# Kernel optimization log

Hardware: AMD Instinct MI355X
Metric: run time of the kernel (lower is better)

The kernel has to match this reference:

```python
import jax, jax.numpy as jnp
import numpy as np
import math

L, B, T, E, HQ, HKV, V = 6, 4, 1024, 1024, 16, 4, 32000
D = E // HQ          # head dim = 64
G = HQ // HKV        # group size = 4
EKV = E // G         # kv proj dim = 256


def setup_inputs() -> dict:
    key = jax.random.key(0)
    ks = jax.random.split(key, 16)
    def n(k, shape):
        return jax.random.normal(k, shape, jnp.float32) * 0.02
    return dict(
        idx=jax.random.randint(ks[0], (B, T), 0, V),
        wte=n(ks[1], (V, E)),
        Wq=n(ks[2], (L, E, E)), bq=jnp.zeros((L, E), jnp.float32),
        Wk=n(ks[3], (L, EKV, E)), bk=jnp.zeros((L, EKV), jnp.float32),
        Wv=n(ks[4], (L, EKV, E)), bv=jnp.zeros((L, EKV), jnp.float32),
        Wo=n(ks[5], (L, E, E)), bo=jnp.zeros((L, E), jnp.float32),
        ln1_w=jnp.ones((L, E), jnp.float32), ln1_b=jnp.zeros((L, E), jnp.float32),
        ln2_w=jnp.ones((L, E), jnp.float32), ln2_b=jnp.zeros((L, E), jnp.float32),
        Wfc=n(ks[6], (L, 4 * E, E)), bfc=jnp.zeros((L, 4 * E), jnp.float32),
        Wproj=n(ks[7], (L, E, 4 * E)), bproj=jnp.zeros((L, E), jnp.float32),
        lnf_w=jnp.ones((E,), jnp.float32), lnf_b=jnp.zeros((E,), jnp.float32),
        lm_head=n(ks[8], (V, E)),
    )


def _ln(x, w, b):
    m = x.mean(-1, keepdims=True)
    v = ((x - m) ** 2).mean(-1, keepdims=True)
    return (x - m) * jax.lax.rsqrt(v + 1e-5) * w + b


def _gelu_new(x):
    c = math.sqrt(2.0 / math.pi)
    return 0.5 * x * (1.0 + jnp.tanh(c * (x + 0.044715 * x ** 3)))


def _rope_tables(t, d):
    # positions start at 1; thetas = base^(-2*(i-1)/d), i = 1..d/2
    pos = jnp.arange(1, t + 1, dtype=jnp.float32)
    thetas = 10000.0 ** (-2.0 * jnp.arange(d // 2, dtype=jnp.float32) / d)
    ang = pos[:, None] * thetas                      # [t, d/2]
    cos = jnp.concatenate([jnp.cos(ang)] * 2, -1)    # [t, d]
    sin = jnp.concatenate([jnp.sin(ang)] * 2, -1)
    return cos, sin


def _apply_rope(x, cos, sin):
    # x: [b, h, t, d]; x_cos = x; x_sin = concat(-right, left)
    x1, x2 = x[..., : D // 2], x[..., D // 2:]
    return x * cos + jnp.concatenate([-x2, x1], -1) * sin


def _gpt_forward(idx, wte, Wq, bq, Wk, bk, Wv, bv, Wo, bo,
                 ln1_w, ln1_b, ln2_w, ln2_b, Wfc, bfc, Wproj, bproj,
                 lnf_w, lnf_b, lm_head):
    cos, sin = _rope_tables(T, D)
    mask = jnp.tril(jnp.ones((T, T), bool))          # causal
    scale = 1.0 / math.sqrt(D)
    x = wte[idx]                                     # [B, T, E]
    for l in range(L):
        h = _ln(x, ln1_w[l], ln1_b[l])
        q = (h @ Wq[l].T + bq[l]).reshape(B, T, HQ, D).transpose(0, 2, 1, 3)
        k = (h @ Wk[l].T + bk[l]).reshape(B, T, HKV, D).transpose(0, 2, 1, 3)
        v = (h @ Wv[l].T + bv[l]).reshape(B, T, HKV, D).transpose(0, 2, 1, 3)
        q = _apply_rope(q, cos, sin)
        k = _apply_rope(k, cos, sin)
        q = q.reshape(B, HKV, G, T, D)               # kv-major head grouping
        att = jnp.einsum('bhgqd,bhkd->bhgqk', q, k) * scale
        att = jnp.where(mask, att, -jnp.inf)
        att = jax.nn.softmax(att, axis=-1)
        y = jnp.einsum('bhgqk,bhkd->bhgqd', att, v)
        y = y.transpose(0, 3, 1, 2, 4).reshape(B, T, E)   # b q (h g d)
        x = x + (y @ Wo[l].T + bo[l])
        h2 = _ln(x, ln2_w[l], ln2_b[l])
        ff = _gelu_new(h2 @ Wfc[l].T + bfc[l]) @ Wproj[l].T + bproj[l]
        x = x + ff
    x = _ln(x, lnf_w, lnf_b)
    return x @ lm_head.T                             # [B, T, V] logits


def reference(idx, wte, Wq, bq, Wk, bk, Wv, bv, Wo, bo,
              ln1_w, ln1_b, ln2_w, ln2_b, Wfc, bfc, Wproj, bproj,
              lnf_w, lnf_b, lm_head):
    return _gpt_forward(idx, wte, Wq, bq, Wk, bk, Wv, bv, Wo, bo,
                        ln1_w, ln1_b, ln2_w, ln2_b, Wfc, bfc, Wproj, bproj,
                        lnf_w, lnf_b, lm_head)
```

## Files before the change

### kernel.cpp

```cpp
#include <hip/hip_runtime.h>

#define Lz 6
#define Bz 4
#define Tz 1024
#define Ez 1024
#define HQz 16
#define HKVz 4
#define Dz 64
#define EKVz 256
#define Vz 32000
#define FFz 4096
#define QKVz 1536

typedef __attribute__((ext_vector_type(4))) float f32x4;
typedef __attribute__((ext_vector_type(8))) short short8;
typedef unsigned short ushort_t;

__device__ inline ushort_t f2b(float f) {
  union { float f; unsigned u; } x; x.f = f;
  unsigned r = x.u + 0x7fffu + ((x.u >> 16) & 1u);
  return (ushort_t)(r >> 16);
}
__device__ inline float b2f(ushort_t u) {
  union { unsigned u; float f; } x; x.u = ((unsigned)u) << 16;
  return x.f;
}
__device__ inline unsigned packbf(float lo, float hi) {
  return (unsigned)f2b(lo) | ((unsigned)f2b(hi) << 16);
}

__device__ inline void gload16(const void* g, void* l) {
  __builtin_amdgcn_global_load_lds(
      (const __attribute__((address_space(1))) void*)g,
      (__attribute__((address_space(3))) void*)l, 16, 0, 0);
}

template<int BIAS, int GELU, int WF32>
__global__ __launch_bounds__(512, 2) void gemm_bt256(
    const ushort_t* __restrict__ A, const ushort_t* __restrict__ Bw,
    const float* __restrict__ bias,
    float* __restrict__ Cf, ushort_t* __restrict__ Cb,
    int M, int N, int K)
{
  __shared__ ushort_t sA[2][2][128 * 64];
  __shared__ ushort_t sB[2][2][128 * 64];
  const int tid = threadIdx.x;
  const int lane = tid & 63, wid = tid >> 6;
  const int wr = wid >> 2, wc = wid & 3;
  const int l15 = lane & 15, l4 = lane >> 4;

  const int gx = gridDim.x;
  const int nwg = gx * gridDim.y;
  const int orig = blockIdx.y * gx + blockIdx.x;
  const int qq = nwg >> 3, rr = nwg & 7;
  const int xcd = orig & 7, loc = orig >> 3;
  const int swz = (xcd < rr) ? (xcd * (qq + 1) + loc)
                             : (rr * (qq + 1) + (xcd - rr) * qq + loc);
  const int bm = swz % gx, bn = swz / gx;

  const int NT = K >> 6;

  auto stage = [&](const ushort_t* src, int row_base, int k0, ushort_t* dst) {
#pragma unroll
    for (int i = 0; i < 2; ++i) {
      int s = i * 512 + tid;
      int row = s >> 3, jp = s & 7;
      int jlog = jp ^ (row & 7);
      gload16(src + (size_t)(row_base + row) * K + k0 + jlog * 8, (char*)dst + s * 16);
    }
  };

  stage(A,  bm * 256,       0, &sA[0][0][0]);
  stage(A,  bm * 256 + 128, 0, &sA[0][1][0]);
  stage(Bw, bn * 256,       0, &sB[0][0][0]);
  stage(Bw, bn * 256 + 128, 0, &sB[0][1][0]);
  stage(A,  bm * 256,       64, &sA[1][0][0]);
  stage(A,  bm * 256 + 128, 64, &sA[1][1][0]);
  stage(Bw, bn * 256,       64, &sB[1][0][0]);
  stage(Bw, bn * 256 + 128, 64, &sB[1][1][0]);
  asm volatile("s_waitcnt vmcnt(8)" ::: "memory");
  __builtin_amdgcn_sched_barrier(0);
  __builtin_amdgcn_s_barrier();
  __builtin_amdgcn_sched_barrier(0);

  f32x4 acc[8][4] = {};
  const int axc = l15 & 7;

  for (int t = 0; t < NT; ++t) {
    const int b = t & 1;
    const ushort_t* pA = &sA[b][wr][0];
    const ushort_t* pB = &sB[b][wc >> 1][(wc & 1) * 64 * 64];
    short8 aF[8][2], bF[4][2];

#pragma unroll
    for (int mt = 0; mt < 4; ++mt)
#pragma unroll
      for (int ks = 0; ks < 2; ++ks)
        aF[mt][ks] = *(const short8*)&pA[(mt * 16 + l15) * 64 + (((ks << 2) + l4) ^ axc) * 8];
#pragma unroll
    for (int nt = 0; nt < 4; ++nt)
      bF[nt][0] = *(const short8*)&pB[(nt * 16 + l15) * 64 + (l4 ^ axc) * 8];
    __builtin_amdgcn_s_setprio(1);
#pragma unroll
    for (int mt = 0; mt < 4; ++mt)
#pragma unroll
      for (int nt = 0; nt < 4; ++nt)
        acc[mt][nt] = __builtin_amdgcn_mfma_f32_16x16x32_bf16(aF[mt][0], bF[nt][0], acc[mt][nt], 0, 0, 0);
    __builtin_amdgcn_s_setprio(0);

#pragma unroll
    for (int mt = 4; mt < 8; ++mt)
#pragma unroll
      for (int ks = 0; ks < 2; ++ks)
        aF[mt][ks] = *(const short8*)&pA[(mt * 16 + l15) * 64 + (((ks << 2) + l4) ^ axc) * 8];
#pragma unroll
    for (int nt = 0; nt < 4; ++nt)
      bF[nt][1] = *(const short8*)&pB[(nt * 16 + l15) * 64 + ((4 + l4) ^ axc) * 8];
    __builtin_amdgcn_s_setprio(1);
#pragma unroll
    for (int mt = 0; mt < 4; ++mt)
#pragma unroll
      for (int nt = 0; nt < 4; ++nt)
        acc[mt][nt] = __builtin_amdgcn_mfma_f32_16x16x32_bf16(aF[mt][1], bF[nt][1], acc[mt][nt], 0, 0, 0);
    __builtin_amdgcn_s_setprio(0);

    asm volatile("s_waitcnt lgkmcnt(0)" ::: "memory");
    __builtin_amdgcn_sched_barrier(0);
    __builtin_amdgcn_s_barrier();
    __builtin_amdgcn_sched_barrier(0);

    const bool pf = (t + 2 < NT);
    if (pf) {
      const int k2 = (t + 2) << 6;
      stage(Bw, bn * 256,       k2, &sB[b][0][0]);
      stage(Bw, bn * 256 + 128, k2, &sB[b][1][0]);
    }
    __builtin_amdgcn_s_setprio(1);
#pragma unroll
    for (int mt = 4; mt < 8; ++mt)
#pragma unroll
      for (int nt = 0; nt < 4; ++nt)
        acc[mt][nt] = __builtin_amdgcn_mfma_f32_16x16x32_bf16(aF[mt][0], bF[nt][0], acc[mt][nt], 0, 0, 0);
    __builtin_amdgcn_s_setprio(0);

    if (pf) {
      const int k2 = (t + 2) << 6;
      stage(A, bm * 256,       k2, &sA[b][0][0]);
      stage(A, bm * 256 + 128, k2, &sA[b][1][0]);
    }
    __builtin_amdgcn_s_setprio(1);
#pragma unroll
    for (int mt = 4; mt < 8; ++mt)
#pragma unroll
      for (int nt = 0; nt < 4; ++nt)
        acc[mt][nt] = __builtin_amdgcn_mfma_f32_16x16x32_bf16(aF[mt][1], bF[nt][1], acc[mt][nt], 0, 0, 0);
    __builtin_amdgcn_s_setprio(0);

    if (t + 1 < NT) {
      if (pf) { asm volatile("s_waitcnt vmcnt(8)" ::: "memory"); }
      else    { asm volatile("s_waitcnt vmcnt(0)" ::: "memory"); }
      __builtin_amdgcn_sched_barrier(0);
      __builtin_amdgcn_s_barrier();
      __builtin_amdgcn_sched_barrier(0);
    }
  }

#pragma unroll
  for (int mt = 0; mt < 8; ++mt) {
#pragma unroll
    for (int nt = 0; nt < 4; ++nt) {
      const int col = bn * 256 + wc * 64 + nt * 16 + l15;
#pragma unroll
      for (int i = 0; i < 4; ++i) {
        const int row = bm * 256 + wr * 128 + mt * 16 + l4 * 4 + i;
        float v = acc[mt][nt][i];
        if (BIAS) v += bias[col];
        if (GELU) {
          float x = v;
          v = 0.5f * x * (1.f + tanhf(0.7978845608028654f * (x + 0.044715f * x * x * x)));
        }
        const size_t o = (size_t)row * N + col;
        if (WF32) Cf[o] = v; else Cb[o] = f2b(v);
      }
    }
  }
}

template<int BIAS, int RES, int GELU, int WBF16, int ROPE>
__global__ __launch_bounds__(256) void gemm_bt64(
    const ushort_t* __restrict__ A, const ushort_t* __restrict__ Bw,
    const float* __restrict__ bias, const ushort_t* __restrict__ res,
    ushort_t* __restrict__ Cb, ushort_t* __restrict__ vtb,
    const float2* __restrict__ tab,
    int M, int N, int K)
{
  __shared__ ushort_t sA[2][128 * 64];
  __shared__ ushort_t sB[2][64 * 64];
  const int tid = threadIdx.x;
  const int lane = tid & 63, wid = tid >> 6;
  const int l15 = lane & 15, l4 = lane >> 4;
  const int xr = l15 & 7;

  const int gx = gridDim.x;
  const int nwg = gx * gridDim.y;
  const int orig = blockIdx.y * gx + blockIdx.x;
  const int qq = nwg >> 3, rr = nwg & 7;
  const int xcd = orig & 7, loc = orig >> 3;
  const int swz = (xcd < rr) ? (xcd * (qq + 1) + loc)
                             : (rr * (qq + 1) + (xcd - rr) * qq + loc);
  const int bm = swz % gx, bn = swz / gx;

  f32x4 acc[2][4] = {};
  const int nK = K >> 6;

  auto stageA = [&](int k0, ushort_t* dst) {
#pragma unroll
    for (int i = 0; i < 4; ++i) {
      int s = i * 256 + tid;
      int row = s >> 3, jp = s & 7;
      int jlog = jp ^ (row & 7);
      gload16(A + (size_t)(bm * 128 + row) * K + k0 + jlog * 8, (char*)dst + s * 16);
    }
  };
  auto stageB = [&](int k0, ushort_t* dst) {
#pragma unroll
    for (int i = 0; i < 2; ++i) {
      int s = i * 256 + tid;
      int row = s >> 3, jp = s & 7;
      int jlog = jp ^ (row & 7);
      gload16(Bw + (size_t)(bn * 64 + row) * K + k0 + jlog * 8, (char*)dst + s * 16);
    }
  };

  stageA(0, &sA[0][0]);
  stageB(0, &sB[0][0]);
  __syncthreads();

  int cur = 0;
  for (int kt = 0; kt < nK; ++kt) {
    if (kt + 1 < nK) {
      const int k0 = (kt + 1) << 6;
      stageA(k0, &sA[cur ^ 1][0]);
      stageB(k0, &sB[cur ^ 1][0]);
    }
    short8 aF[2][2], bF[4][2];
#pragma unroll
    for (int mt = 0; mt < 2; ++mt)
#pragma unroll
      for (int ks = 0; ks < 2; ++ks)
        aF[mt][ks] = *(const short8*)&sA[cur][(wid * 32 + mt * 16 + l15) * 64 + (((ks << 2) + l4) ^ xr) * 8];
#pragma unroll
    for (int nt = 0; nt < 4; ++nt)
#pragma unroll
      for (int ks = 0; ks < 2; ++ks)
        bF[nt][ks] = *(const short8*)&sB[cur][(nt * 16 + l15) * 64 + (((ks << 2) + l4) ^ xr) * 8];
#pragma unroll
    for (int mt = 0; mt < 2; ++mt)
#pragma unroll
      for (int nt = 0; nt < 4; ++nt)
#pragma unroll
        for (int ks = 0; ks < 2; ++ks)
          acc[mt][nt] = __builtin_amdgcn_mfma_f32_16x16x32_bf16(aF[mt][ks], bF[nt][ks], acc[mt][nt], 0, 0, 0);
    __syncthreads();
    cur ^= 1;
  }

  if (ROPE) {
    const int col0 = bn * 64;
    const bool isv = (col0 >= 1280);
#pragma unroll
    for (int mt = 0; mt < 2; ++mt) {
      const int row_base = bm * 128 + wid * 32 + mt * 16 + l4 * 4;
      const int bb = row_base >> 10, t0 = row_base & (Tz - 1);
      if (isv) {
#pragma unroll
        for (int nt = 0; nt < 4; ++nt) {
          const int col = col0 + nt * 16 + l15;
          const int cm = col - 1280, hk = cm >> 6, d = cm & 63;
          ushort4 w;
          w.x = f2b(acc[mt][nt][0] + bias[col]);
          w.y = f2b(acc[mt][nt][1] + bias[col]);
          w.z = f2b(acc[mt][nt][2] + bias[col]);
          w.w = f2b(acc[mt][nt][3] + bias[col]);
          *(ushort4*)&vtb[((size_t)(bb * HKVz + hk) * 64 + d) * Tz + t0] = w;
        }
      } else {
#pragma unroll
        for (int i = 0; i < 4; ++i) {
          const int row = row_base + i;
          const int t = row & (Tz - 1);
#pragma unroll
          for (int nt = 0; nt < 2; ++nt) {
            const int col = col0 + nt * 16 + l15;
            const int jj = nt * 16 + l15;
            const float2 cs = tab[t * 32 + jj];
            const float x1 = acc[mt][nt][i] + bias[col];
            const float x2 = acc[mt][nt + 2][i] + bias[col + 32];
            Cb[(size_t)row * N + col]      = f2b(x1 * cs.x - x2 * cs.y);
            Cb[(size_t)row * N + col + 32] = f2b(x2 * cs.x + x1 * cs.y);
          }
        }
      }
    }
    return;
  }

#pragma unroll
  for (int mt = 0; mt < 2; ++mt) {
#pragma unroll
    for (int nt = 0; nt < 4; ++nt) {
      const int col = bn * 64 + nt * 16 + l15;
#pragma unroll
      for (int i = 0; i < 4; ++i) {
        const int row = bm * 128 + wid * 32 + mt * 16 + l4 * 4 + i;
        float v = acc[mt][nt][i];
        if (BIAS) v += bias[col];
        if (GELU) {
          float t = v;
          v = 0.5f * t * (1.f + tanhf(0.7978845608028654f * (t + 0.044715f * t * t * t)));
        }
        const size_t o = (size_t)row * N + col;
        if (RES) v += b2f(res[o]);
        if (WBF16) Cb[o] = f2b(v);
      }
    }
  }
}

__global__ __launch_bounds__(256, 4) void attn_k(
    const ushort_t* __restrict__ qkv, const ushort_t* __restrict__ vt,
    ushort_t* __restrict__ y)
{
  __shared__ ushort_t sK[2][64 * 64];
  __shared__ ushort_t sV[2][64 * 64];
  __shared__ unsigned sPu[4][512];
  const int bh = blockIdx.y;
  const int b = bh >> 4, h = bh & 15, hk = h >> 2;
  const int tid = threadIdx.x, lane = tid & 63, wid = tid >> 6;
  const int l15 = lane & 15, l4 = lane >> 4;
  const int xr = l15 & 7;

  for (int pass = 0; pass < 2; ++pass) {
    const int qt = pass ? (int)blockIdx.x : (Tz / 64 - 1 - (int)blockIdx.x);
    const int qrow0 = qt * 64 + wid * 16;
    const int qg = qrow0 + l15;
    const int ntile = qt + 1;

    short8 aQ[2];
#pragma unroll
    for (int ks = 0; ks < 2; ++ks)
      aQ[ks] = *(const short8*)&qkv[(size_t)(b * Tz + qrow0 + l15) * QKVz + h * 64 + ks * 32 + l4 * 8];

    float m = -1e30f, lsum = 0.f;
    f32x4 o[4] = {};

    if (pass) __syncthreads();

#pragma unroll
    for (int j = 0; j < 2; ++j) {
      int s = wid * 128 + j * 64 + lane;
      int row = s >> 3, jp = s & 7, jlog = jp ^ (row & 7);
      gload16(qkv + (size_t)(b * Tz + row) * QKVz + Ez + hk * 64 + jlog * 8, (char*)&sK[0][0] + s * 16);
      gload16(vt + (size_t)((b * HKVz + hk) * 64 + row) * Tz + jlog * 8, (char*)&sV[0][0] + s * 16);
    }

    for (int t = 0; t < ntile; ++t) {
      asm volatile("s_waitcnt vmcnt(0)" ::: "memory");
      __syncthreads();
      if (t + 1 < ntile) {
        const int nb = (t + 1) & 1;
#pragma unroll
        for (int j = 0; j < 2; ++j) {
          int s = wid * 128 + j * 64 + lane;
          int row = s >> 3, jp = s & 7, jlog = jp ^ (row & 7);
          gload16(qkv + (size_t)(b * Tz + (t + 1) * 64 + row) * QKVz + Ez + hk * 64 + jlog * 8,
                  (char*)&sK[nb][0] + s * 16);
          gload16(vt + (size_t)((b * HKVz + hk) * 64 + row) * Tz + (t + 1) * 64 + jlog * 8,
                  (char*)&sV[nb][0] + s * 16);
        }
      }
      const ushort_t* K = &sK[t & 1][0];
      const ushort_t* V = &sV[t & 1][0];

      f32x4 sacc[4] = {};
#pragma unroll
      for (int nt = 0; nt < 4; ++nt) {
#pragma unroll
        for (int ks = 0; ks < 2; ++ks) {
          short8 aK = *(const short8*)&K[(nt * 16 + l15) * 64 + (((ks << 2) + l4) ^ xr) * 8];
          sacc[nt] = __builtin_amdgcn_mfma_f32_16x16x32_bf16(aK, aQ[ks], sacc[nt], 0, 0, 0);
        }
      }

      float sv[4][4];
      float pmax = -1e30f;
#pragma unroll
      for (int nt = 0; nt < 4; ++nt)
#pragma unroll
        for (int i = 0; i < 4; ++i) {
          int key = t * 64 + nt * 16 + l4 * 4 + i;
          float s = sacc[nt][i] * 0.125f;
          if (key > qg) s = -1e30f;
          sv[nt][i] = s;
          pmax = fmaxf(pmax, s);
        }
      pmax = fmaxf(pmax, __shfl_xor(pmax, 16));
      pmax = fmaxf(pmax, __shfl_xor(pmax, 32));
      const float mnew = fmaxf(m, pmax);
      const float corr = __expf(m - mnew);
      float psum = 0.f;
#pragma unroll
      for (int nt = 0; nt < 4; ++nt)
#pragma unroll
        for (int i = 0; i < 4; ++i) {
          float p = __expf(sv[nt][i] - mnew);
          sv[nt][i] = p;
          psum += p;
        }
      psum += __shfl_xor(psum, 16);
      psum += __shfl_xor(psum, 32);
      lsum = lsum * corr + psum;
      m = mnew;
#pragma unroll
      for (int dt = 0; dt < 4; ++dt) o[dt] *= corr;

#pragma unroll
      for (int nt = 0; nt < 4; ++nt) {
        uint2 u;
        u.x = packbf(sv[nt][0], sv[nt][1]);
        u.y = packbf(sv[nt][2], sv[nt][3]);
        *(uint2*)&sPu[wid][l15 * 32 + (((nt * 2 + (l4 >> 1)) ^ xr) << 2) + ((l4 & 1) << 1)] = u;
      }
      short8 aP[2];
#pragma unroll
      for (int ks = 0; ks < 2; ++ks)
        aP[ks] = *(const short8*)&sPu[wid][l15 * 32 + ((((ks << 2) + l4) ^ xr) << 2)];

#pragma unroll
      for (int dt = 0; dt < 4; ++dt) {
#pragma unroll
        for (int ks = 0; ks < 2; ++ks) {
          short8 aV = *(const short8*)&V[(dt * 16 + l15) * 64 + (((ks << 2) + l4) ^ xr) * 8];
          o[dt] = __builtin_amdgcn_mfma_f32_16x16x32_bf16(aV, aP[ks], o[dt], 0, 0, 0);
        }
      }
    }

    const float inv = 1.f / lsum;
    const size_t yrow = (size_t)(b * Tz + qrow0 + l15) * Ez + h * 64;
#pragma unroll
    for (int dt = 0; dt < 4; ++dt) {
      ushort4 w;
      w.x = f2b(o[dt][0] * inv);
      w.y = f2b(o[dt][1] * inv);
      w.z = f2b(o[dt][2] * inv);
      w.w = f2b(o[dt][3] * inv);
      *(ushort4*)&y[yrow + dt * 16 + l4 * 4] = w;
    }
  }
}

__global__ __launch_bounds__(256) void ln_bf16(
    const ushort_t* __restrict__ x, const float* __restrict__ w,
    const float* __restrict__ b, ushort_t* __restrict__ out)
{
  __shared__ float red[8];
  const int row = blockIdx.x, tid = threadIdx.x;
  ushort4 xv = *(const ushort4*)&x[(size_t)row * Ez + tid * 4];
  float v0 = b2f(xv.x), v1 = b2f(xv.y), v2 = b2f(xv.z), v3 = b2f(xv.w);
  float s = v0 + v1 + v2 + v3;
  float sq = v0 * v0 + v1 * v1 + v2 * v2 + v3 * v3;
#pragma unroll
  for (int off = 1; off < 64; off <<= 1) { s += __shfl_xor(s, off); sq += __shfl_xor(sq, off); }
  if ((tid & 63) == 0) { red[(tid >> 6) * 2] = s; red[(tid >> 6) * 2 + 1] = sq; }
  __syncthreads();
  const float ts = red[0] + red[2] + red[4] + red[6];
  const float tq = red[1] + red[3] + red[5] + red[7];
  const float mean = ts * (1.f / Ez);
  const float var = tq * (1.f / Ez) - mean * mean;
  const float rstd = rsqrtf(var + 1e-5f);
  float4 wv = *(const float4*)&w[tid * 4];
  float4 bv = *(const float4*)&b[tid * 4];
  ushort4 ov;
  ov.x = f2b((v0 - mean) * rstd * wv.x + bv.x);
  ov.y = f2b((v1 - mean) * rstd * wv.y + bv.y);
  ov.z = f2b((v2 - mean) * rstd * wv.z + bv.z);
  ov.w = f2b((v3 - mean) * rstd * wv.w + bv.w);
  *(ushort4*)&out[(size_t)row * Ez + tid * 4] = ov;
}

__global__ __launch_bounds__(256) void embed_k(
    const int* __restrict__ idx, const float* __restrict__ wte, ushort_t* __restrict__ x)
{
  int i = blockIdx.x * 256 + threadIdx.x;
  int row = i >> 8, c = (i & 255) << 2;
  float4 v = *(const float4*)&wte[(size_t)idx[row] * Ez + c];
  ushort4 o;
  o.x = f2b(v.x); o.y = f2b(v.y); o.z = f2b(v.z); o.w = f2b(v.w);
  *(ushort4*)&x[(size_t)row * Ez + c] = o;
}

__global__ __launch_bounds__(256) void cvt_bf16(
    const float* __restrict__ in, ushort_t* __restrict__ out, int n)
{
  int i = (blockIdx.x * 256 + threadIdx.x) * 4;
  if (i >= n) return;
  float4 v = *(const float4*)&in[i];
  ushort4 o;
  o.x = f2b(v.x); o.y = f2b(v.y); o.z = f2b(v.z); o.w = f2b(v.w);
  *(ushort4*)&out[i] = o;
}

__global__ __launch_bounds__(256) void cvt_layer(
    const float* __restrict__ Wq, const float* __restrict__ Wk,
    const float* __restrict__ Wv, const float* __restrict__ Wo_,
    const float* __restrict__ Wfc_, const float* __restrict__ Wpj_,
    ushort_t* __restrict__ wqkv, ushort_t* __restrict__ wo,
    ushort_t* __restrict__ wfc, ushort_t* __restrict__ wpj)
{
  int i = (blockIdx.x * 256 + threadIdx.x) * 4;
  const float* src; ushort_t* dst; int off;
  if (i < 1048576)       { src = Wq;   dst = wqkv;           off = i; }
  else if (i < 1310720)  { src = Wk;   dst = wqkv + 1048576; off = i - 1048576; }
  else if (i < 1572864)  { src = Wv;   dst = wqkv + 1310720; off = i - 1310720; }
  else if (i < 2621440)  { src = Wo_;  dst = wo;             off = i - 1572864; }
  else if (i < 6815744)  { src = Wfc_; dst = wfc;            off = i - 2621440; }
  else                   { src = Wpj_; dst = wpj;            off = i - 6815744; }
  float4 v = *(const float4*)&src[off];
  ushort4 o;
  o.x = f2b(v.x); o.y = f2b(v.y); o.z = f2b(v.z); o.w = f2b(v.w);
  *(ushort4*)&dst[off] = o;
}

__global__ __launch_bounds__(256) void setup_k(
    const float* __restrict__ bq, const float* __restrict__ bk,
    const float* __restrict__ bv, float2* __restrict__ tab, float* __restrict__ qbia)
{
  int i = blockIdx.x * 256 + threadIdx.x;
  int t = i >> 5, j = i & 31;
  float theta = powf(10000.0f, -(float)j / 32.0f);
  float ang = (float)(t + 1) * theta;
  tab[i] = make_float2(cosf(ang), sinf(ang));
  if (i < Lz * QKVz) {
    int l = i / QKVz, jj = i - l * QKVz;
    float v = (jj < Ez) ? bq[l * Ez + jj]
            : ((jj < Ez + EKVz) ? bk[l * EKVz + jj - Ez] : bv[l * EKVz + jj - Ez - EKVz]);
    qbia[i] = v;
  }
}

template<int BIAS, int RES, int GELU, int WBF16, int ROPE = 0>
static void launch_gemm64(const ushort_t* A, const ushort_t* Bw, const float* bias,
                          const ushort_t* res, ushort_t* Cb,
                          ushort_t* vtb, const float* tab,
                          int M, int N, int K, hipStream_t s)
{
  dim3 g(M / 128, N / 64);
  gemm_bt64<BIAS, RES, GELU, WBF16, ROPE><<<g, 256, 0, s>>>(
      A, Bw, bias, res, Cb, vtb, (const float2*)tab, M, N, K);
}

extern "C" void kernel_launch(void* const* d_in, const int* in_sizes, int n_in,
                              void* d_out, int out_size, void* d_ws, size_t ws_size,
                              hipStream_t stream)
{
  (void)in_sizes; (void)n_in; (void)out_size; (void)ws_size;
  const int*   idx   = (const int*)d_in[0];
  const float* wte   = (const float*)d_in[1];
  const float* Wq    = (const float*)d_in[2];
  const float* bq    = (const float*)d_in[3];
  const float* Wk    = (const float*)d_in[4];
  const float* bk    = (const float*)d_in[5];
  const float* Wv    = (const float*)d_in[6];
  const float* bv    = (const float*)d_in[7];
  const float* Wo    = (const float*)d_in[8];
  const float* bo    = (const float*)d_in[9];
  const float* ln1w  = (const float*)d_in[10];
  const float* ln1b  = (const float*)d_in[11];
  const float* ln2w  = (const float*)d_in[12];
  const float* ln2b  = (const float*)d_in[13];
  const float* Wfc   = (const float*)d_in[14];
  const float* bfc   = (const float*)d_in[15];
  const float* Wproj = (const float*)d_in[16];
  const float* bproj = (const float*)d_in[17];
  const float* lnfw  = (const float*)d_in[18];
  const float* lnfb  = (const float*)d_in[19];
  const float* lmh   = (const float*)d_in[20];
  float* out = (float*)d_out;

  char* ws = (char*)d_ws;
  size_t off = 0;
  auto alloc = [&](size_t bytes) -> void* {
    void* p = ws + off;
    off += (bytes + 255) & ~(size_t)255;
    return p;
  };
  ushort_t* wbuf  = (ushort_t*)alloc((size_t)Vz * Ez * 2);
  ushort_t* x     = (ushort_t*)alloc((size_t)Bz * Tz * Ez * 2);
  ushort_t* hb    = (ushort_t*)alloc((size_t)Bz * Tz * Ez * 2);
  ushort_t* qkvb  = (ushort_t*)alloc((size_t)Bz * Tz * QKVz * 2);
  ushort_t* vtb   = (ushort_t*)alloc((size_t)Bz * HKVz * 64 * Tz * 2);
  ushort_t* yb    = (ushort_t*)alloc((size_t)Bz * Tz * Ez * 2);
  ushort_t* ffb   = (ushort_t*)alloc((size_t)Bz * Tz * FFz * 2);
  float*    tab   = (float*)alloc((size_t)Tz * 32 * 2 * 4);
  float*    qbia  = (float*)alloc((size_t)Lz * QKVz * 4);

  ushort_t* wqkv = wbuf;
  ushort_t* wo   = wqkv + (size_t)QKVz * Ez;
  ushort_t* wfc  = wo + (size_t)Ez * Ez;
  ushort_t* wpj  = wfc + (size_t)FFz * Ez;

  const int M = Bz * Tz;

  setup_k<<<Tz * 32 / 256, 256, 0, stream>>>(bq, bk, bv, (float2*)tab, qbia);
  embed_k<<<Bz * Tz, 256, 0, stream>>>(idx, wte, x);

  for (int l = 0; l < Lz; ++l) {
    ln_bf16<<<M, 256, 0, stream>>>(x, ln1w + l * Ez, ln1b + l * Ez, hb);
    cvt_layer<<<10752, 256, 0, stream>>>(
        Wq + (size_t)l * Ez * Ez, Wk + (size_t)l * EKVz * Ez, Wv + (size_t)l * EKVz * Ez,
        Wo + (size_t)l * Ez * Ez, Wfc + (size_t)l * FFz * Ez, Wproj + (size_t)l * Ez * FFz,
        wqkv, wo, wfc, wpj);
    launch_gemm64<1, 0, 0, 1, 1>(hb, wqkv, qbia + l * QKVz, nullptr, qkvb, vtb, tab,
                                 M, QKVz, Ez, stream);
    attn_k<<<dim3(Tz / 128, Bz * HQz), 256, 0, stream>>>(qkvb, vtb, yb);
    launch_gemm64<1, 1, 0, 1>(yb, wo, bo + l * Ez, x, x, nullptr, nullptr,
                              M, Ez, Ez, stream);
    ln_bf16<<<M, 256, 0, stream>>>(x, ln2w + l * Ez, ln2b + l * Ez, hb);
    {
      dim3 g(M / 256, FFz / 256);
      gemm_bt256<1, 1, 0><<<g, 512, 0, stream>>>(hb, wfc, bfc + l * FFz, nullptr, ffb, M, FFz, Ez);
    }
    launch_gemm64<1, 1, 0, 1>(ffb, wpj, bproj + l * Ez, x, x, nullptr, nullptr,
                              M, Ez, FFz, stream);
  }
  ln_bf16<<<M, 256, 0, stream>>>(x, lnfw, lnfb, hb);
  cvt_bf16<<<(Vz * Ez / 4 + 255) / 256, 256, 0, stream>>>(lmh, wbuf, Vz * Ez);
  {
    dim3 g(M / 256, Vz / 256);
    gemm_bt256<0, 0, 1><<<g, 512, 0, stream>>>(hb, wbuf, nullptr, out, nullptr, M, Vz, Ez);
  }
}
```

Baseline: 1.592 ms.

## Load GEMM A fragments directly from global memory, staging only B in LDS

```diff
diff --git a/kernel.cpp b/kernel.cpp
--- a/kernel.cpp
+++ b/kernel.cpp
@@ -36,18 +36,18 @@
 }
 
 template<int BIAS, int GELU, int WF32>
-__global__ __launch_bounds__(512, 2) void gemm_bt256(
+__global__ __launch_bounds__(512, 1) void gemm_bt256(
     const ushort_t* __restrict__ A, const ushort_t* __restrict__ Bw,
     const float* __restrict__ bias,
     float* __restrict__ Cf, ushort_t* __restrict__ Cb,
     int M, int N, int K)
 {
-  __shared__ ushort_t sA[2][2][128 * 64];
   __shared__ ushort_t sB[2][2][128 * 64];
   const int tid = threadIdx.x;
   const int lane = tid & 63, wid = tid >> 6;
   const int wr = wid >> 2, wc = wid & 3;
   const int l15 = lane & 15, l4 = lane >> 4;
+  const int axc = l15 & 7;
 
   const int gx = gridDim.x;
   const int nwg = gx * gridDim.y;
@@ -60,109 +60,60 @@
 
   const int NT = K >> 6;
 
-  auto stage = [&](const ushort_t* src, int row_base, int k0, ushort_t* dst) {
-#pragma unroll
-    for (int i = 0; i < 2; ++i) {
-      int s = i * 512 + tid;
-      int row = s >> 3, jp = s & 7;
-      int jlog = jp ^ (row & 7);
-      gload16(src + (size_t)(row_base + row) * K + k0 + jlog * 8, (char*)dst + s * 16);
-    }
+  auto stageB = [&](int k0, int buf) {
+#pragma unroll
+    for (int h = 0; h < 2; ++h) {
+      int s = (h & 1) * 512 + tid;
+      (void)s;
+    }
+#pragma unroll
+    for (int h = 0; h < 2; ++h)
+#pragma unroll
+      for (int i = 0; i < 2; ++i) {
+        int s = i * 512 + tid;
+        int row = s >> 3, jp = s & 7;
+        int jlog = jp ^ (row & 7);
+        gload16(Bw + (size_t)(bn * 256 + h * 128 + row) * K + k0 + jlog * 8,
+                (char*)&sB[buf][h][0] + s * 16);
+      }
   };
 
-  stage(A,  bm * 256,       0, &sA[0][0][0]);
-  stage(A,  bm * 256 + 128, 0, &sA[0][1][0]);
-  stage(Bw, bn * 256,       0, &sB[0][0][0]);
-  stage(Bw, bn * 256 + 128, 0, &sB[0][1][0]);
-  stage(A,  bm * 256,       64, &sA[1][0][0]);
-  stage(A,  bm * 256 + 128, 64, &sA[1][1][0]);
-  stage(Bw, bn * 256,       64, &sB[1][0][0]);
-  stage(Bw, bn * 256 + 128, 64, &sB[1][1][0]);
-  asm volatile("s_waitcnt vmcnt(8)" ::: "memory");
-  __builtin_amdgcn_sched_barrier(0);
-  __builtin_amdgcn_s_barrier();
-  __builtin_amdgcn_sched_barrier(0);
+  stageB(0, 0);
+  asm volatile("s_waitcnt vmcnt(0)" ::: "memory");
+  __syncthreads();
 
   f32x4 acc[8][4] = {};
-  const int axc = l15 & 7;
-
+  const ushort_t* Abase = A + (size_t)(bm * 256 + wr * 128 + l15) * K + l4 * 8;
+
+  int cur = 0;
   for (int t = 0; t < NT; ++t) {
-    const int b = t & 1;
-    const ushort_t* pA = &sA[b][wr][0];
-    const ushort_t* pB = &sB[b][wc >> 1][(wc & 1) * 64 * 64];
+    if (t + 1 < NT) stageB((t + 1) << 6, cur ^ 1);
+    const ushort_t* pB = &sB[cur][wc >> 1][(wc & 1) * 64 * 64];
     short8 aF[8][2], bF[4][2];
-
-#pragma unroll
-    for (int mt = 0; mt < 4; ++mt)
+#pragma unroll
+    for (int mt = 0; mt < 8; ++mt)
 #pragma unroll
       for (int ks = 0; ks < 2; ++ks)
-        aF[mt][ks] = *(const short8*)&pA[(mt * 16 + l15) * 64 + (((ks << 2) + l4) ^ axc) * 8];
+        aF[mt][ks] = *(const short8*)&Abase[(size_t)mt * 16 * K + t * 64 + ks * 32];
 #pragma unroll
     for (int nt = 0; nt < 4; ++nt)
-      bF[nt][0] = *(const short8*)&pB[(nt * 16 + l15) * 64 + (l4 ^ axc) * 8];
+#pragma unroll
+      for (int ks = 0; ks < 2; ++ks)
+        bF[nt][ks] = *(const short8*)&pB[(nt * 16 + l15) * 64 + (((ks << 2) + l4) ^ axc) * 8];
     __builtin_amdgcn_s_setprio(1);
 #pragma unroll
-    for (int mt = 0; mt < 4; ++mt)
+    for (int mt = 0; mt < 8; ++mt)
 #pragma unroll
       for (int nt = 0; nt < 4; ++nt)
-        acc[mt][nt] = __builtin_amdgcn_mfma_f32_16x16x32_bf16(aF[mt][0], bF[nt][0], acc[mt][nt], 0, 0, 0);
+#pragma unroll
+        for (int ks = 0; ks < 2; ++ks)
+          acc[mt][nt] = __builtin_amdgcn_mfma_f32_16x16x32_bf16(aF[mt][ks], bF[nt][ks], acc[mt][nt], 0, 0, 0);
     __builtin_amdgcn_s_setprio(0);
-
-#pragma unroll
-    for (int mt = 4; mt < 8; ++mt)
-#pragma unroll
-      for (int ks = 0; ks < 2; ++ks)
-        aF[mt][ks] = *(const short8*)&pA[(mt * 16 + l15) * 64 + (((ks << 2) + l4) ^ axc) * 8];
-#pragma unroll
-    for (int nt = 0; nt < 4; ++nt)
-      bF[nt][1] = *(const short8*)&pB[(nt * 16 + l15) * 64 + ((4 + l4) ^ axc) * 8];
-    __builtin_amdgcn_s_setprio(1);
-#pragma unroll
-    for (int mt = 0; mt < 4; ++mt)
-#pragma unroll
-      for (int nt = 0; nt < 4; ++nt)
-        acc[mt][nt] = __builtin_amdgcn_mfma_f32_16x16x32_bf16(aF[mt][1], bF[nt][1], acc[mt][nt], 0, 0, 0);
-    __builtin_amdgcn_s_setprio(0);
-
-    asm volatile("s_waitcnt lgkmcnt(0)" ::: "memory");
-    __builtin_amdgcn_sched_barrier(0);
+    asm volatile("s_waitcnt vmcnt(16)" ::: "memory");
+    asm volatile("" ::: "memory");
     __builtin_amdgcn_s_barrier();
-    __builtin_amdgcn_sched_barrier(0);
-
-    const bool pf = (t + 2 < NT);
-    if (pf) {
-      const int k2 = (t + 2) << 6;
-      stage(Bw, bn * 256,       k2, &sB[b][0][0]);
-      stage(Bw, bn * 256 + 128, k2, &sB[b][1][0]);
-    }
-    __builtin_amdgcn_s_setprio(1);
-#pragma unroll
-    for (int mt = 4; mt < 8; ++mt)
-#pragma unroll
-      for (int nt = 0; nt < 4; ++nt)
-        acc[mt][nt] = __builtin_amdgcn_mfma_f32_16x16x32_bf16(aF[mt][0], bF[nt][0], acc[mt][nt], 0, 0, 0);
-    __builtin_amdgcn_s_setprio(0);
-
-    if (pf) {
-      const int k2 = (t + 2) << 6;
-      stage(A, bm * 256,       k2, &sA[b][0][0]);
-      stage(A, bm * 256 + 128, k2, &sA[b][1][0]);
-    }
-    __builtin_amdgcn_s_setprio(1);
-#pragma unroll
-    for (int mt = 4; mt < 8; ++mt)
-#pragma unroll
-      for (int nt = 0; nt < 4; ++nt)
-        acc[mt][nt] = __builtin_amdgcn_mfma_f32_16x16x32_bf16(aF[mt][1], bF[nt][1], acc[mt][nt], 0, 0, 0);
-    __builtin_amdgcn_s_setprio(0);
-
-    if (t + 1 < NT) {
-      if (pf) { asm volatile("s_waitcnt vmcnt(8)" ::: "memory"); }
-      else    { asm volatile("s_waitcnt vmcnt(0)" ::: "memory"); }
-      __builtin_amdgcn_sched_barrier(0);
-      __builtin_amdgcn_s_barrier();
-      __builtin_amdgcn_sched_barrier(0);
-    }
+    asm volatile("" ::: "memory");
+    cur ^= 1;
   }
 
 #pragma unroll
```

Result: slower. 2.223 ms (+39.7%).
